# Performance work log

Hardware: AMD Instinct MI355X
Metric: run time of the kernel (lower is better)

## Reference

```python
import jax, jax.numpy as jnp
import numpy as np

B, N, CQ, CKV, CP = 4, 1024, 128, 64, 16
H, NB = 4, 3
D = CQ // H  # 32 per-head dim
NQ, NK = 32, 128
CENTRES = 15.5 + 32.0 * np.arange(N // NQ)  # subset centres covering all atoms


def _ln(x, eps=1e-5):
    m = jnp.mean(x, axis=-1, keepdims=True)
    v = jnp.var(x, axis=-1, keepdims=True)
    return (x - m) * jax.lax.rsqrt(v + eps)


def _adaln(a, s, s_gamma, w_gate, w_skip):
    # AF3 AdaLN: a normalized without affine, modulated by conditioning s
    a_n = _ln(a)
    s_n = _ln(s) * s_gamma
    return jax.nn.sigmoid(s_n @ w_gate) * a_n + s_n @ w_skip


def _local_bias():
    # sequence-local block mask (union over subset centres), Algorithm 7
    idx = jnp.arange(N, dtype=jnp.float32)
    cen = jnp.asarray(CENTRES, dtype=jnp.float32)
    lcond = jnp.abs(idx[None, :] - cen[:, None]) < NQ / 2  # [C, N] query window
    mcond = jnp.abs(idx[None, :] - cen[:, None]) < NK / 2  # [C, N] key window
    cond = jnp.any(lcond[:, :, None] & mcond[:, None, :], axis=0)  # [N, N]
    return jnp.where(cond, 0.0, -1e10)


def _forward(q, c, p, attn_s_gamma, attn_gate_w, attn_skip_w, attn_wq, attn_bq,
             attn_wk, attn_wv, attn_lnz_g, attn_lnz_b, attn_wb, attn_wgate,
             attn_wo, attn_ws_out, attn_bs_out, trans_s_gamma, trans_gate_w,
             trans_skip_w, trans_w1, trans_w2, trans_wout, trans_ws_out,
             trans_bs_out):
    beta = _local_bias()  # [N, N]
    inv_sqrt_d = 1.0 / np.sqrt(D)
    a = q
    for i in range(NB):  # 3 structurally distinct blocks
        # --- AttentionPairBias (AF3 Alg 24) ---
        ah = _adaln(a, c, attn_s_gamma[i], attn_gate_w[i], attn_skip_w[i])
        qh = (ah @ attn_wq[i] + attn_bq[i]).reshape(B, N, H, D)
        kh = (ah @ attn_wk[i]).reshape(B, N, H, D)
        vh = (ah @ attn_wv[i]).reshape(B, N, H, D)
        zb = (_ln(p) * attn_lnz_g[i] + attn_lnz_b[i]) @ attn_wb[i]  # [B,N,N,H]
        bias = jnp.transpose(zb, (0, 3, 1, 2)) + beta[None, None]  # [B,H,N,N]
        scores = jnp.einsum('bqhd,bkhd->bhqk', qh, kh) * inv_sqrt_d + bias
        w = jax.nn.softmax(scores, axis=-1)
        o = jnp.einsum('bhqk,bkhd->bqhd', w, vh)
        g = jax.nn.sigmoid((ah @ attn_wgate[i]).reshape(B, N, H, D))
        o = (g * o).reshape(B, N, CQ) @ attn_wo[i]
        attn_out = jax.nn.sigmoid(c @ attn_ws_out[i] + attn_bs_out[i]) * o
        # --- ConditionedTransitionBlock (AF3 Alg 25, n=2 SwiGLU) ---
        t = _adaln(a, c, trans_s_gamma[i], trans_gate_w[i], trans_skip_w[i])
        bm = jax.nn.silu(t @ trans_w1[i]) * (t @ trans_w2[i])
        t_out = jax.nn.sigmoid(c @ trans_ws_out[i] + trans_bs_out[i]) * (bm @ trans_wout[i])
        # AF3 Alg 23: a <- attn_out + transition(a, s)
        a = attn_out + t_out
    return a


def setup_inputs() -> dict:
    key = jax.random.key(0)
    ks = iter(jax.random.split(key, 64))

    def rnd(shape, scale=0.02):
        return jax.random.normal(next(ks), shape, dtype=jnp.float32) * scale

    return {
        'q': jax.random.normal(next(ks), (B, N, CQ), dtype=jnp.float32),
        'c': jax.random.normal(next(ks), (B, N, CKV), dtype=jnp.float32),
        'p': jax.random.normal(next(ks), (B, N, N, CP), dtype=jnp.float32),
        'attn_s_gamma': jnp.ones((NB, CKV), jnp.float32),
        'attn_gate_w': rnd((NB, CKV, CQ)),
        'attn_skip_w': rnd((NB, CKV, CQ)),
        'attn_wq': rnd((NB, CQ, CQ)),
        'attn_bq': jnp.zeros((NB, CQ), jnp.float32),
        'attn_wk': rnd((NB, CQ, CQ)),
        'attn_wv': rnd((NB, CQ, CQ)),
        'attn_lnz_g': jnp.ones((NB, CP), jnp.float32),
        'attn_lnz_b': jnp.zeros((NB, CP), jnp.float32),
        'attn_wb': rnd((NB, CP, H)),
        'attn_wgate': rnd((NB, CQ, CQ)),
        'attn_wo': rnd((NB, CQ, CQ)),
        'attn_ws_out': rnd((NB, CKV, CQ)),
        'attn_bs_out': jnp.full((NB, CQ), -2.0, jnp.float32),
        'trans_s_gamma': jnp.ones((NB, CKV), jnp.float32),
        'trans_gate_w': rnd((NB, CKV, CQ)),
        'trans_skip_w': rnd((NB, CKV, CQ)),
        'trans_w1': rnd((NB, CQ, 2 * CQ)),
        'trans_w2': rnd((NB, CQ, 2 * CQ)),
        'trans_wout': rnd((NB, 2 * CQ, CQ)),
        'trans_ws_out': rnd((NB, CKV, CQ)),
        'trans_bs_out': jnp.full((NB, CQ), -2.0, jnp.float32),
    }


def reference(q, c, p, attn_s_gamma, attn_gate_w, attn_skip_w, attn_wq, attn_bq,
              attn_wk, attn_wv, attn_lnz_g, attn_lnz_b, attn_wb, attn_wgate,
              attn_wo, attn_ws_out, attn_bs_out, trans_s_gamma, trans_gate_w,
              trans_skip_w, trans_w1, trans_w2, trans_wout, trans_ws_out,
              trans_bs_out):
    return _forward(q, c, p, attn_s_gamma, attn_gate_w, attn_skip_w, attn_wq,
                    attn_bq, attn_wk, attn_wv, attn_lnz_g, attn_lnz_b, attn_wb,
                    attn_wgate, attn_wo, attn_ws_out, attn_bs_out,
                    trans_s_gamma, trans_gate_w, trans_skip_w, trans_w1,
                    trans_w2, trans_wout, trans_ws_out, trans_bs_out)
```

## Files before the change

### kernel.cpp

```cpp
#include <hip/hip_runtime.h>
#include <math.h>

#define NB_ 3
#define B_ 4
#define N_ 1024
#define CQ_ 128
#define CKV_ 64
#define CP_ 16
#define H_ 4
#define D_ 32
#define R_ (B_*N_)
#define KW_ 128

__device__ __forceinline__ float sigmoidf_(float x) {
    return 1.0f / (1.0f + __expf(-x));
}

#define AN_OFF 0
#define SA_OFF 1056
#define ST_OFF 1600
#define CR_OFF 2144
#define TH_OFF 2688
#define SCR_OFF 3744
#define SMEM_F (3744 + 6336)

__global__ __launch_bounds__(512, 4) void k_pre(
    const float* __restrict__ a, const float* __restrict__ c,
    const float* __restrict__ a_sg, const float* __restrict__ a_gw,
    const float* __restrict__ a_sw, const float* __restrict__ a_wso,
    const float* __restrict__ a_bso,
    const float* __restrict__ t_sg, const float* __restrict__ t_gw,
    const float* __restrict__ t_sw, const float* __restrict__ t_wso,
    const float* __restrict__ t_bso,
    const float* __restrict__ wq, const float* __restrict__ bq,
    const float* __restrict__ wk, const float* __restrict__ wv,
    const float* __restrict__ wg,
    const float* __restrict__ w1, const float* __restrict__ w2,
    float* __restrict__ qh, float* __restrict__ kh,
    float* __restrict__ vh, float* __restrict__ gh,
    float* __restrict__ bm,
    float* __restrict__ asig, float* __restrict__ tsig)
{
    __shared__ float smem[SMEM_F];
    const int t = threadIdx.x;
    const int base = blockIdx.x * 8;

    {
        const int rloc = t >> 6, li = t & 63;
        const int row = base + rloc;
        float2 av = *(const float2*)(a + row * 128 + li * 2);
        float s = av.x + av.y;
        float ss = av.x * av.x + av.y * av.y;
        float cv = c[row * 64 + li];
        float cs = cv, css = cv * cv;
        #pragma unroll
        for (int m = 1; m < 64; m <<= 1) {
            s += __shfl_xor(s, m);
            ss += __shfl_xor(ss, m);
            cs += __shfl_xor(cs, m);
            css += __shfl_xor(css, m);
        }
        const float am = s * (1.0f / 128.0f);
        const float ars = rsqrtf(ss * (1.0f / 128.0f) - am * am + 1e-5f);
        const float cm = cs * (1.0f / 64.0f);
        const float crs = rsqrtf(css * (1.0f / 64.0f) - cm * cm + 1e-5f);
        smem[AN_OFF + rloc * 132 + li * 2]     = (av.x - am) * ars;
        smem[AN_OFF + rloc * 132 + li * 2 + 1] = (av.y - am) * ars;
        const float cn = (cv - cm) * crs;
        smem[SA_OFF + rloc * 68 + li] = cn * a_sg[li];
        smem[ST_OFF + rloc * 68 + li] = cn * t_sg[li];
        smem[CR_OFF + rloc * 68 + li] = cv;
    }
    __syncthreads();

    const int wave = t >> 6;
    const int lane = t & 63;
    const int ig = lane >> 4;
    const int jc = lane & 15;
    const int c0 = jc * 8;
    const int r0 = ig * 2, r1 = ig * 2 + 1;

    if (wave < 6) {
        const float* W;
        const float* xs;
        switch (wave) {
            case 0: W = a_gw;  xs = smem + SA_OFF; break;
            case 1: W = a_sw;  xs = smem + SA_OFF; break;
            case 2: W = t_gw;  xs = smem + ST_OFF; break;
            case 3: W = t_sw;  xs = smem + ST_OFF; break;
            case 4: W = a_wso; xs = smem + CR_OFF; break;
            default: W = t_wso; xs = smem + CR_OFF; break;
        }
        W += c0;
        float acc0[8], acc1[8];
        #pragma unroll
        for (int e = 0; e < 8; e++) { acc0[e] = 0.f; acc1[e] = 0.f; }
        for (int kk = 0; kk < 64; kk += 4) {
            float4 x40 = *(const float4*)(xs + r0 * 68 + kk);
            float4 x41 = *(const float4*)(xs + r1 * 68 + kk);
            #pragma unroll
            for (int q = 0; q < 4; q++) {
                const float4 wlo = *(const float4*)(W + (kk + q) * 128);
                const float4 whi = *(const float4*)(W + (kk + q) * 128 + 4);
                const float xa = ((const float*)&x40)[q];
                const float xb = ((const float*)&x41)[q];
                acc0[0] += xa * wlo.x; acc0[1] += xa * wlo.y;
                acc0[2] += xa * wlo.z; acc0[3] += xa * wlo.w;
                acc0[4] += xa * whi.x; acc0[5] += xa * whi.y;
                acc0[6] += xa * whi.z; acc0[7] += xa * whi.w;
                acc1[0] += xb * wlo.x; acc1[1] += xb * wlo.y;
                acc1[2] += xb * wlo.z; acc1[3] += xb * wlo.w;
                acc1[4] += xb * whi.x; acc1[5] += xb * whi.y;
                acc1[6] += xb * whi.z; acc1[7] += xb * whi.w;
            }
        }
        float* sc = smem + SCR_OFF + wave * 1056;
        *(float4*)(sc + r0 * 132 + c0)     = make_float4(acc0[0], acc0[1], acc0[2], acc0[3]);
        *(float4*)(sc + r0 * 132 + c0 + 4) = make_float4(acc0[4], acc0[5], acc0[6], acc0[7]);
        *(float4*)(sc + r1 * 132 + c0)     = make_float4(acc1[0], acc1[1], acc1[2], acc1[3]);
        *(float4*)(sc + r1 * 132 + c0 + 4) = make_float4(acc1[4], acc1[5], acc1[6], acc1[7]);
    }
    __syncthreads();

    #pragma unroll
    for (int i2 = 0; i2 < 2; i2++) {
        const int e = t + i2 * 512;
        const int r = e >> 7, cc = e & 127;
        const float* sc = smem + SCR_OFF + r * 132 + cc;
        const float anv = smem[AN_OFF + r * 132 + cc];
        const float ahv = sigmoidf_(sc[0]) * anv + sc[1056];
        const float thv = sigmoidf_(sc[2 * 1056]) * anv + sc[3 * 1056];
        smem[AN_OFF + r * 132 + cc] = ahv;
        smem[TH_OFF + r * 132 + cc] = thv;
        const int idx = (base + r) * 128 + cc;
        asig[idx] = sigmoidf_(sc[4 * 1056] + a_bso[cc]);
        tsig[idx] = sigmoidf_(sc[5 * 1056] + t_bso[cc]);
    }
    __syncthreads();

    {
        const float* W;
        const float* xs;
        int ldw, sel2 = 0, cb = 0;
        if (wave < 4) {
            W = (wave == 0 ? wq : wave == 1 ? wk : wave == 2 ? wv : wg) + c0;
            xs = smem + AN_OFF;
            ldw = 128;
        } else {
            const int u = (wave - 4) * 128 + c0;
            sel2 = u >> 8; cb = u & 255;
            W = (sel2 ? w2 : w1) + cb;
            xs = smem + TH_OFF;
            ldw = 256;
        }
        float acc0[8], acc1[8];
        #pragma unroll
        for (int e = 0; e < 8; e++) {
            const float init = (wave == 0) ? bq[c0 + e] : 0.f;
            acc0[e] = init; acc1[e] = init;
        }
        for (int kk = 0; kk < 128; kk += 4) {
            float4 x40 = *(const float4*)(xs + r0 * 132 + kk);
            float4 x41 = *(const float4*)(xs + r1 * 132 + kk);
            #pragma unroll
            for (int q = 0; q < 4; q++) {
                const float4 wlo = *(const float4*)(W + (kk + q) * ldw);
                const float4 whi = *(const float4*)(W + (kk + q) * ldw + 4);
                const float xa = ((const float*)&x40)[q];
                const float xb = ((const float*)&x41)[q];
                acc0[0] += xa * wlo.x; acc0[1] += xa * wlo.y;
                acc0[2] += xa * wlo.z; acc0[3] += xa * wlo.w;
                acc0[4] += xa * whi.x; acc0[5] += xa * whi.y;
                acc0[6] += xa * whi.z; acc0[7] += xa * whi.w;
                acc1[0] += xb * wlo.x; acc1[1] += xb * wlo.y;
                acc1[2] += xb * wlo.z; acc1[3] += xb * wlo.w;
                acc1[4] += xb * whi.x; acc1[5] += xb * whi.y;
                acc1[6] += xb * whi.z; acc1[7] += xb * whi.w;
            }
        }
        if (wave < 4) {
            float* dst = (wave == 0 ? qh : wave == 1 ? kh : wave == 2 ? vh : gh);
            if (wave == 3) {
                #pragma unroll
                for (int e = 0; e < 8; e++) {
                    acc0[e] = sigmoidf_(acc0[e]);
                    acc1[e] = sigmoidf_(acc1[e]);
                }
            }
            *(float4*)(dst + (base + r0) * 128 + c0)     = make_float4(acc0[0], acc0[1], acc0[2], acc0[3]);
            *(float4*)(dst + (base + r0) * 128 + c0 + 4) = make_float4(acc0[4], acc0[5], acc0[6], acc0[7]);
            *(float4*)(dst + (base + r1) * 128 + c0)     = make_float4(acc1[0], acc1[1], acc1[2], acc1[3]);
            *(float4*)(dst + (base + r1) * 128 + c0 + 4) = make_float4(acc1[4], acc1[5], acc1[6], acc1[7]);
        } else {
            float* bsc = smem + SCR_OFF + sel2 * 2080;
            *(float4*)(bsc + r0 * 260 + cb)     = make_float4(acc0[0], acc0[1], acc0[2], acc0[3]);
            *(float4*)(bsc + r0 * 260 + cb + 4) = make_float4(acc0[4], acc0[5], acc0[6], acc0[7]);
            *(float4*)(bsc + r1 * 260 + cb)     = make_float4(acc1[0], acc1[1], acc1[2], acc1[3]);
            *(float4*)(bsc + r1 * 260 + cb + 4) = make_float4(acc1[4], acc1[5], acc1[6], acc1[7]);
        }
    }
    __syncthreads();

    #pragma unroll
    for (int i2 = 0; i2 < 4; i2++) {
        const int e = t + i2 * 512;
        const int r = e >> 8, cc = e & 255;
        const float a1 = smem[SCR_OFF + r * 260 + cc];
        const float a2 = smem[SCR_OFF + 2080 + r * 260 + cc];
        bm[(base + r) * 256 + cc] = a1 * sigmoidf_(a1) * a2;
    }
}

__global__ __launch_bounds__(256) void k_zbias(
    const float* __restrict__ p,
    const float* __restrict__ lnz_g, const float* __restrict__ lnz_b,
    const float* __restrict__ wb, float* __restrict__ zb)
{
    const int tid = blockIdx.x * 256 + threadIdx.x;
    const int kk = tid & 127;
    const int n = (tid >> 7) & 1023;
    const int b = tid >> 17;
    const int row = b * N_ + n;
    const int k = ((n >> 5) << 5) - 48 + kk;

    if (k < 0 || k >= N_) {
        #pragma unroll
        for (int blk = 0; blk < NB_; blk++) {
            float* zo = zb + ((size_t)(blk * R_ + row) * H_) * KW_ + kk;
            #pragma unroll
            for (int h = 0; h < H_; h++) zo[h * KW_] = -1e10f;
        }
        return;
    }
    const float* pp = p + ((size_t)row * N_ + k) * CP_;
    float pv[16];
    float4 p0 = *(const float4*)(pp);
    float4 p1 = *(const float4*)(pp + 4);
    float4 p2 = *(const float4*)(pp + 8);
    float4 p3 = *(const float4*)(pp + 12);
    pv[0]=p0.x; pv[1]=p0.y; pv[2]=p0.z; pv[3]=p0.w;
    pv[4]=p1.x; pv[5]=p1.y; pv[6]=p1.z; pv[7]=p1.w;
    pv[8]=p2.x; pv[9]=p2.y; pv[10]=p2.z; pv[11]=p2.w;
    pv[12]=p3.x; pv[13]=p3.y; pv[14]=p3.z; pv[15]=p3.w;
    float s = 0.f, ss = 0.f;
    #pragma unroll
    for (int i = 0; i < 16; i++) { s += pv[i]; ss += pv[i] * pv[i]; }
    const float m = s * (1.0f / 16.0f);
    const float rs = rsqrtf(ss * (1.0f / 16.0f) - m * m + 1e-5f);

    #pragma unroll
    for (int blk = 0; blk < NB_; blk++) {
        const float* g = lnz_g + blk * 16;
        const float* bb = lnz_b + blk * 16;
        const float* w = wb + blk * 64;
        float z0 = 0.f, z1 = 0.f, z2 = 0.f, z3 = 0.f;
        #pragma unroll
        for (int cp = 0; cp < 16; cp++) {
            const float val = (pv[cp] - m) * rs * g[cp] + bb[cp];
            z0 += val * w[cp * 4 + 0];
            z1 += val * w[cp * 4 + 1];
            z2 += val * w[cp * 4 + 2];
            z3 += val * w[cp * 4 + 3];
        }
        float* zo = zb + ((size_t)(blk * R_ + row) * H_) * KW_ + kk;
        zo[0] = z0; zo[KW_] = z1; zo[2 * KW_] = z2; zo[3 * KW_] = z3;
    }
}

__global__ __launch_bounds__(256) void k_attn(
    const float* __restrict__ qh, const float* __restrict__ kh,
    const float* __restrict__ vh, const float* __restrict__ gh,
    const float* __restrict__ zb, float* __restrict__ og)
{
    __shared__ float kT[32][136];
    __shared__ float vs[128][36];
    __shared__ float wsm[32][132];

    const int t = threadIdx.x;
    const int qb = blockIdx.x, h = blockIdx.y, b = blockIdx.z;
    const int k0 = qb * 32 - 48;

    #pragma unroll
    for (int i = 0; i < 16; i++) {
        const int e = t + i * 256;
        const int kk = e >> 5, d = e & 31;
        const int kg = k0 + kk;
        float kvv = 0.f, vvv = 0.f;
        if (kg >= 0 && kg < N_) {
            const int addr = (b * N_ + kg) * 128 + h * 32 + d;
            kvv = kh[addr]; vvv = vh[addr];
        }
        kT[d][kk] = kvv;
        vs[kk][d] = vvv;
    }

    const int q = t >> 3, j = t & 7;
    const int n = qb * 32 + q;
    const float* qrow = qh + (b * N_ + n) * 128 + h * 32;
    float4 qf[8];
    #pragma unroll
    for (int dq = 0; dq < 8; dq++) qf[dq] = *(const float4*)(qrow + dq * 4);
    const float* zrow = zb + ((size_t)(b * N_ + n) * H_ + h) * KW_;
    float4 zf[4];
    #pragma unroll
    for (int g4 = 0; g4 < 4; g4++) zf[g4] = *(const float4*)(zrow + j * 16 + g4 * 4);
    __syncthreads();

    float4 acc[4];
    #pragma unroll
    for (int g4 = 0; g4 < 4; g4++) acc[g4] = make_float4(0.f, 0.f, 0.f, 0.f);
    const float* qfs = (const float*)qf;
    for (int d = 0; d < 32; d++) {
        const float qd = qfs[d];
        #pragma unroll
        for (int g4 = 0; g4 < 4; g4++) {
            const float4 k4 = *(const float4*)&kT[d][j * 16 + g4 * 4];
            acc[g4].x += qd * k4.x; acc[g4].y += qd * k4.y;
            acc[g4].z += qd * k4.z; acc[g4].w += qd * k4.w;
        }
    }
    const float scale = 0.1767766952966369f;
    float fr[16];
    #pragma unroll
    for (int g4 = 0; g4 < 4; g4++) {
        fr[g4*4+0] = zf[g4].x + acc[g4].x * scale;
        fr[g4*4+1] = zf[g4].y + acc[g4].y * scale;
        fr[g4*4+2] = zf[g4].z + acc[g4].z * scale;
        fr[g4*4+3] = zf[g4].w + acc[g4].w * scale;
    }
    float mx = fr[0];
    #pragma unroll
    for (int i = 1; i < 16; i++) mx = fmaxf(mx, fr[i]);
    #pragma unroll
    for (int mk = 1; mk < 8; mk <<= 1) mx = fmaxf(mx, __shfl_xor(mx, mk));
    float sum = 0.f;
    #pragma unroll
    for (int i = 0; i < 16; i++) { fr[i] = __expf(fr[i] - mx); sum += fr[i]; }
    #pragma unroll
    for (int mk = 1; mk < 8; mk <<= 1) sum += __shfl_xor(sum, mk);
    const float rinv = 1.0f / sum;
    #pragma unroll
    for (int g4 = 0; g4 < 4; g4++)
        #pragma unroll
        for (int mm = 0; mm < 4; mm++)
            wsm[q][j * 16 + g4 * 4 + mm] = fr[g4 * 4 + mm] * rinv;
    __syncthreads();

    const int q2 = t >> 3, dg = t & 7;
    float4 o = make_float4(0.f, 0.f, 0.f, 0.f);
    for (int kk = 0; kk < 128; kk++) {
        const float wv_ = wsm[q2][kk];
        const float4 v4 = *(const float4*)&vs[kk][dg * 4];
        o.x += wv_ * v4.x; o.y += wv_ * v4.y;
        o.z += wv_ * v4.z; o.w += wv_ * v4.w;
    }
    const int n2 = qb * 32 + q2;
    const int addr = (b * N_ + n2) * 128 + h * 32 + dg * 4;
    const float4 g4v = *(const float4*)(gh + addr);
    float4 outv;
    outv.x = o.x * g4v.x; outv.y = o.y * g4v.y;
    outv.z = o.z * g4v.z; outv.w = o.w * g4v.w;
    *(float4*)(og + addr) = outv;
}

__global__ __launch_bounds__(256, 4) void k_combine(
    const float* __restrict__ og, const float* __restrict__ bm,
    const float* __restrict__ wo, const float* __restrict__ wout,
    const float* __restrict__ asig, const float* __restrict__ tsig,
    float* __restrict__ out)
{
    __shared__ float scr[4 * 1056];
    const int t = threadIdx.x;
    const int base = blockIdx.x * 8;
    const int wave = t >> 6, lane = t & 63;
    const int ig = lane >> 4, jc = lane & 15;
    const int c0 = jc * 8;
    const int r0 = ig * 2, r1 = ig * 2 + 1;

    float acc0[8], acc1[8];
    #pragma unroll
    for (int e = 0; e < 8; e++) { acc0[e] = 0.f; acc1[e] = 0.f; }

    if (wave < 2) {
        const float* W = wo + c0;
        const float* X = og + base * 128;
        const int kbeg = wave * 64;
        for (int kk = kbeg; kk < kbeg + 64; kk += 4) {
            float4 x40 = *(const float4*)(X + r0 * 128 + kk);
            float4 x41 = *(const float4*)(X + r1 * 128 + kk);
            #pragma unroll
            for (int q = 0; q < 4; q++) {
                const float4 wlo = *(const float4*)(W + (kk + q) * 128);
                const float4 whi = *(const float4*)(W + (kk + q) * 128 + 4);
                const float xa = ((const float*)&x40)[q];
                const float xb = ((const float*)&x41)[q];
                acc0[0] += xa * wlo.x; acc0[1] += xa * wlo.y;
                acc0[2] += xa * wlo.z; acc0[3] += xa * wlo.w;
                acc0[4] += xa * whi.x; acc0[5] += xa * whi.y;
                acc0[6] += xa * whi.z; acc0[7] += xa * whi.w;
                acc1[0] += xb * wlo.x; acc1[1] += xb * wlo.y;
                acc1[2] += xb * wlo.z; acc1[3] += xb * wlo.w;
                acc1[4] += xb * whi.x; acc1[5] += xb * whi.y;
                acc1[6] += xb * whi.z; acc1[7] += xb * whi.w;
            }
        }
    } else {
        const float* W = wout + c0;
        const float* X = bm + base * 256;
        const int kbeg = (wave - 2) * 128;
        for (int kk = kbeg; kk < kbeg + 128; kk += 4) {
            float4 x40 = *(const float4*)(X + r0 * 256 + kk);
            float4 x41 = *(const float4*)(X + r1 * 256 + kk);
            #pragma unroll
            for (int q = 0; q < 4; q++) {
                const float4 wlo = *(const float4*)(W + (kk + q) * 128);
                const float4 whi = *(const float4*)(W + (kk + q) * 128 + 4);
                const float xa = ((const float*)&x40)[q];
                const float xb = ((const float*)&x41)[q];
                acc0[0] += xa * wlo.x; acc0[1] += xa * wlo.y;
                acc0[2] += xa * wlo.z; acc0[3] += xa * wlo.w;
                acc0[4] += xa * whi.x; acc0[5] += xa * whi.y;
                acc0[6] += xa * whi.z; acc0[7] += xa * whi.w;
                acc1[0] += xb * wlo.x; acc1[1] += xb * wlo.y;
                acc1[2] += xb * wlo.z; acc1[3] += xb * wlo.w;
                acc1[4] += xb * whi.x; acc1[5] += xb * whi.y;
                acc1[6] += xb * whi.z; acc1[7] += xb * whi.w;
            }
        }
    }
    float* sc = scr + wave * 1056;
    *(float4*)(sc + r0 * 132 + c0)     = make_float4(acc0[0], acc0[1], acc0[2], acc0[3]);
    *(float4*)(sc + r0 * 132 + c0 + 4) = make_float4(acc0[4], acc0[5], acc0[6], acc0[7]);
    *(float4*)(sc + r1 * 132 + c0)     = make_float4(acc1[0], acc1[1], acc1[2], acc1[3]);
    *(float4*)(sc + r1 * 132 + c0 + 4) = make_float4(acc1[4], acc1[5], acc1[6], acc1[7]);
    __syncthreads();

    #pragma unroll
    for (int i2 = 0; i2 < 4; i2++) {
        const int e = t + i2 * 256;
        const int r = e >> 7, cc = e & 127;
        const float* s = scr + r * 132 + cc;
        const int idx = (base + r) * 128 + cc;
        out[idx] = asig[idx] * (s[0] + s[1056]) + tsig[idx] * (s[2112] + s[3168]);
    }
}

extern "C" void kernel_launch(void* const* d_in, const int* in_sizes, int n_in,
                              void* d_out, int out_size, void* d_ws, size_t ws_size,
                              hipStream_t stream)
{
    const float* q        = (const float*)d_in[0];
    const float* c        = (const float*)d_in[1];
    const float* p        = (const float*)d_in[2];
    const float* a_sg_all = (const float*)d_in[3];
    const float* a_gw_all = (const float*)d_in[4];
    const float* a_sw_all = (const float*)d_in[5];
    const float* wq_all   = (const float*)d_in[6];
    const float* bq_all   = (const float*)d_in[7];
    const float* wk_all   = (const float*)d_in[8];
    const float* wv_all   = (const float*)d_in[9];
    const float* lnzg_all = (const float*)d_in[10];
    const float* lnzb_all = (const float*)d_in[11];
    const float* wb_all   = (const float*)d_in[12];
    const float* wgt_all  = (const float*)d_in[13];
    const float* wo_all   = (const float*)d_in[14];
    const float* awso_all = (const float*)d_in[15];
    const float* abso_all = (const float*)d_in[16];
    const float* t_sg_all = (const float*)d_in[17];
    const float* t_gw_all = (const float*)d_in[18];
    const float* t_sw_all = (const float*)d_in[19];
    const float* w1_all   = (const float*)d_in[20];
    const float* w2_all   = (const float*)d_in[21];
    const float* wout_all = (const float*)d_in[22];
    const float* twso_all = (const float*)d_in[23];
    const float* tbso_all = (const float*)d_in[24];

    float* ws = (float*)d_ws;
    const size_t RC = (size_t)R_ * CQ_;
    float* qh   = ws;
    float* kh   = ws + RC;
    float* vh   = ws + 2 * RC;
    float* gh   = ws + 3 * RC;
    float* bmb  = ws + 4 * RC;
    float* asig = ws + 6 * RC;
    float* tsig = ws + 7 * RC;
    float* abuf = ws + 8 * RC;
    float* ogb  = ws + 9 * RC;
    float* zbb  = ws + 10 * RC;

    k_zbias<<<dim3(B_ * N_ * KW_ / 256), dim3(256), 0, stream>>>(
        p, lnzg_all, lnzb_all, wb_all, zbb);

    const float* acur = q;
    for (int blk = 0; blk < NB_; blk++) {
        k_pre<<<dim3(R_ / 8), dim3(512), 0, stream>>>(
            acur, c,
            a_sg_all + blk * CKV_, a_gw_all + blk * CKV_ * CQ_,
            a_sw_all + blk * CKV_ * CQ_, awso_all + blk * CKV_ * CQ_,
            abso_all + blk * CQ_,
            t_sg_all + blk * CKV_, t_gw_all + blk * CKV_ * CQ_,
            t_sw_all + blk * CKV_ * CQ_, twso_all + blk * CKV_ * CQ_,
            tbso_all + blk * CQ_,
            wq_all + blk * CQ_ * CQ_, bq_all + blk * CQ_,
            wk_all + blk * CQ_ * CQ_, wv_all + blk * CQ_ * CQ_,
            wgt_all + blk * CQ_ * CQ_,
            w1_all + blk * CQ_ * 2 * CQ_, w2_all + blk * CQ_ * 2 * CQ_,
            qh, kh, vh, gh, bmb, asig, tsig);
        k_attn<<<dim3(N_ / 32, H_, B_), dim3(256), 0, stream>>>(
            qh, kh, vh, gh, zbb + (size_t)blk * R_ * H_ * KW_, ogb);
        float* outp = (blk == NB_ - 1) ? (float*)d_out : abuf;
        k_combine<<<dim3(R_ / 8), dim3(256), 0, stream>>>(
            ogb, bmb, wo_all + blk * CQ_ * CQ_, wout_all + blk * 2 * CQ_ * CQ_,
            asig, tsig, outp);
        acur = abuf;
    }
}
```

Baseline: 648.5 us.

## Fuse output combine with next block's prep, fold z-bias into first prep

The separate z-bias kernel is folded into a new first-block prep kernel. Each block's output projection and gating now run in one kernel, k_cp, with the next block's AdaLN and QKV/transition projections, so the intermediate activation never round-trips through global memory and fewer kernels are launched. The attention kernel moves to 512 threads with a flattened grid, stages Q in shared memory, loads K/V as vectors, and splits the weighted-V reduction across lane pairs. In exchange, the output projection in k_cp is a simple per-row loop, and bm, asig and tsig are read and rewritten in place under restrict pointers.

New measurement: 686.4 us. +5.8%, slower.

```diff
diff --git a/kernel.cpp b/kernel.cpp
--- a/kernel.cpp
+++ b/kernel.cpp
@@ -24,8 +24,9 @@
 #define SCR_OFF 3744
 #define SMEM_F (3744 + 6336)
 
-__global__ __launch_bounds__(512, 4) void k_pre(
-    const float* __restrict__ a, const float* __restrict__ c,
+__device__ __forceinline__ void pre_body(
+    float2 av, float* smem, int base,
+    const float* __restrict__ c,
     const float* __restrict__ a_sg, const float* __restrict__ a_gw,
     const float* __restrict__ a_sw, const float* __restrict__ a_wso,
     const float* __restrict__ a_bso,
@@ -41,14 +42,10 @@
     float* __restrict__ bm,
     float* __restrict__ asig, float* __restrict__ tsig)
 {
-    __shared__ float smem[SMEM_F];
     const int t = threadIdx.x;
-    const int base = blockIdx.x * 8;
-
     {
         const int rloc = t >> 6, li = t & 63;
         const int row = base + rloc;
-        float2 av = *(const float2*)(a + row * 128 + li * 2);
         float s = av.x + av.y;
         float ss = av.x * av.x + av.y * av.y;
         float cv = c[row * 64 + li];
@@ -99,11 +96,11 @@
             float4 x40 = *(const float4*)(xs + r0 * 68 + kk);
             float4 x41 = *(const float4*)(xs + r1 * 68 + kk);
             #pragma unroll
-            for (int q = 0; q < 4; q++) {
-                const float4 wlo = *(const float4*)(W + (kk + q) * 128);
-                const float4 whi = *(const float4*)(W + (kk + q) * 128 + 4);
-                const float xa = ((const float*)&x40)[q];
-                const float xb = ((const float*)&x41)[q];
+            for (int qq = 0; qq < 4; qq++) {
+                const float4 wlo = *(const float4*)(W + (kk + qq) * 128);
+                const float4 whi = *(const float4*)(W + (kk + qq) * 128 + 4);
+                const float xa = ((const float*)&x40)[qq];
+                const float xb = ((const float*)&x41)[qq];
                 acc0[0] += xa * wlo.x; acc0[1] += xa * wlo.y;
                 acc0[2] += xa * wlo.z; acc0[3] += xa * wlo.w;
                 acc0[4] += xa * whi.x; acc0[5] += xa * whi.y;
@@ -163,11 +160,11 @@
             float4 x40 = *(const float4*)(xs + r0 * 132 + kk);
             float4 x41 = *(const float4*)(xs + r1 * 132 + kk);
             #pragma unroll
-            for (int q = 0; q < 4; q++) {
-                const float4 wlo = *(const float4*)(W + (kk + q) * ldw);
-                const float4 whi = *(const float4*)(W + (kk + q) * ldw + 4);
-                const float xa = ((const float*)&x40)[q];
-                const float xb = ((const float*)&x41)[q];
+            for (int qq = 0; qq < 4; qq++) {
+                const float4 wlo = *(const float4*)(W + (kk + qq) * ldw);
+                const float4 whi = *(const float4*)(W + (kk + qq) * ldw + 4);
+                const float xa = ((const float*)&x40)[qq];
+                const float xb = ((const float*)&x41)[qq];
                 acc0[0] += xa * wlo.x; acc0[1] += xa * wlo.y;
                 acc0[2] += xa * wlo.z; acc0[3] += xa * wlo.w;
                 acc0[4] += xa * whi.x; acc0[5] += xa * whi.y;
@@ -211,237 +208,255 @@
     }
 }
 
-__global__ __launch_bounds__(256) void k_zbias(
+__global__ __launch_bounds__(512, 4) void k_pre0(
+    const float* __restrict__ a, const float* __restrict__ c,
     const float* __restrict__ p,
     const float* __restrict__ lnz_g, const float* __restrict__ lnz_b,
-    const float* __restrict__ wb, float* __restrict__ zb)
+    const float* __restrict__ wb, float* __restrict__ zb,
+    const float* __restrict__ a_sg, const float* __restrict__ a_gw,
+    const float* __restrict__ a_sw, const float* __restrict__ a_wso,
+    const float* __restrict__ a_bso,
+    const float* __restrict__ t_sg, const float* __restrict__ t_gw,
+    const float* __restrict__ t_sw, const float* __restrict__ t_wso,
+    const float* __restrict__ t_bso,
+    const float* __restrict__ wq, const float* __restrict__ bq,
+    const float* __restrict__ wk, const float* __restrict__ wv,
+    const float* __restrict__ wg,
+    const float* __restrict__ w1, const float* __restrict__ w2,
+    float* __restrict__ qh, float* __restrict__ kh,
+    float* __restrict__ vh, float* __restrict__ gh,
+    float* __restrict__ bm,
+    float* __restrict__ asig, float* __restrict__ tsig)
 {
-    const int tid = blockIdx.x * 256 + threadIdx.x;
-    const int kk = tid & 127;
-    const int n = (tid >> 7) & 1023;
-    const int b = tid >> 17;
-    const int row = b * N_ + n;
-    const int k = ((n >> 5) << 5) - 48 + kk;
-
-    if (k < 0 || k >= N_) {
-        #pragma unroll
-        for (int blk = 0; blk < NB_; blk++) {
-            float* zo = zb + ((size_t)(blk * R_ + row) * H_) * KW_ + kk;
+    __shared__ float smem[SMEM_F];
+    const int t = threadIdx.x;
+    const int base = blockIdx.x * 8;
+
+    #pragma unroll
+    for (int i = 0; i < 2; i++) {
+        const int e = t + i * 512;
+        const int r = e >> 7, kk = e & 127;
+        const int row = base + r;
+        const int n = row & 1023;
+        const int k = ((n >> 5) << 5) - 48 + kk;
+        if (k < 0 || k >= N_) {
             #pragma unroll
-            for (int h = 0; h < H_; h++) zo[h * KW_] = -1e10f;
-        }
+            for (int blk = 0; blk < NB_; blk++) {
+                float* zo = zb + ((size_t)(blk * R_ + row) * H_) * KW_ + kk;
+                #pragma unroll
+                for (int h = 0; h < H_; h++) zo[h * KW_] = -1e10f;
+            }
+        } else {
+            const float* pp = p + ((size_t)row * N_ + k) * CP_;
+            float pv[16];
+            float4 p0 = *(const float4*)(pp);
+            float4 p1 = *(const float4*)(pp + 4);
+            float4 p2 = *(const float4*)(pp + 8);
+            float4 p3 = *(const float4*)(pp + 12);
+            pv[0]=p0.x; pv[1]=p0.y; pv[2]=p0.z; pv[3]=p0.w;
+            pv[4]=p1.x; pv[5]=p1.y; pv[6]=p1.z; pv[7]=p1.w;
+            pv[8]=p2.x; pv[9]=p2.y; pv[10]=p2.z; pv[11]=p2.w;
+            pv[12]=p3.x; pv[13]=p3.y; pv[14]=p3.z; pv[15]=p3.w;
+            float s = 0.f, ss = 0.f;
+            #pragma unroll
+            for (int ii = 0; ii < 16; ii++) { s += pv[ii]; ss += pv[ii] * pv[ii]; }
+            const float m = s * (1.0f / 16.0f);
+            const float rs = rsqrtf(ss * (1.0f / 16.0f) - m * m + 1e-5f);
+            #pragma unroll
+            for (int blk = 0; blk < NB_; blk++) {
+                const float* g = lnz_g + blk * 16;
+                const float* bb = lnz_b + blk * 16;
+                const float* w = wb + blk * 64;
+                float z0 = 0.f, z1 = 0.f, z2 = 0.f, z3 = 0.f;
+                #pragma unroll
+                for (int cp = 0; cp < 16; cp++) {
+                    const float val = (pv[cp] - m) * rs * g[cp] + bb[cp];
+                    z0 += val * w[cp * 4 + 0];
+                    z1 += val * w[cp * 4 + 1];
+                    z2 += val * w[cp * 4 + 2];
+                    z3 += val * w[cp * 4 + 3];
+                }
+                float* zo = zb + ((size_t)(blk * R_ + row) * H_) * KW_ + kk;
+                zo[0] = z0; zo[KW_] = z1; zo[2 * KW_] = z2; zo[3 * KW_] = z3;
+            }
+        }
+    }
+
+    float2 av = *(const float2*)(a + (base + (t >> 6)) * 128 + (t & 63) * 2);
+    pre_body(av, smem, base, c, a_sg, a_gw, a_sw, a_wso, a_bso,
+             t_sg, t_gw, t_sw, t_wso, t_bso, wq, bq, wk, wv, wg, w1, w2,
+             qh, kh, vh, gh, bm, asig, tsig);
+}
+
+__global__ __launch_bounds__(512, 4) void k_cp(
+    const float* __restrict__ og, const float* __restrict__ bm_in,
+    const float* __restrict__ wo, const float* __restrict__ wout,
+    const float* __restrict__ asig_in, const float* __restrict__ tsig_in,
+    float* __restrict__ out_final, int final_,
+    const float* __restrict__ c,
+    const float* __restrict__ a_sg, const float* __restrict__ a_gw,
+    const float* __restrict__ a_sw, const float* __restrict__ a_wso,
+    const float* __restrict__ a_bso,
+    const float* __restrict__ t_sg, const float* __restrict__ t_gw,
+    const float* __restrict__ t_sw, const float* __restrict__ t_wso,
+    const float* __restrict__ t_bso,
+    const float* __restrict__ wq, const float* __restrict__ bq,
+    const float* __restrict__ wk, const float* __restrict__ wv,
+    const float* __restrict__ wg,
+    const float* __restrict__ w1, const float* __restrict__ w2,
+    float* __restrict__ qh, float* __restrict__ kh,
+    float* __restrict__ vh, float* __restrict__ gh,
+    float* __restrict__ bm,
+    float* __restrict__ asig, float* __restrict__ tsig)
+{
+    __shared__ float smem[SMEM_F];
+    float* ogs = smem + SCR_OFF;
+    float* bms = smem + SCR_OFF + 1056;
+    const int t = threadIdx.x;
+    const int base = blockIdx.x * 8;
+
+    if (t < 256) {
+        const int r = t >> 5, c4 = t & 31;
+        *(float4*)(ogs + r * 132 + c4 * 4) =
+            *(const float4*)(og + (base + r) * 128 + c4 * 4);
+    }
+    {
+        const int r = t >> 6, c4 = t & 63;
+        *(float4*)(bms + r * 260 + c4 * 4) =
+            *(const float4*)(bm_in + (base + r) * 256 + c4 * 4);
+    }
+    __syncthreads();
+
+    const int w = t >> 6, l = t & 63;
+    const int row = base + w;
+    float2 acc1 = make_float2(0.f, 0.f), acc2 = make_float2(0.f, 0.f);
+    for (int k = 0; k < 128; k++) {
+        const float x = ogs[w * 132 + k];
+        const float2 wv = *(const float2*)(wo + k * 128 + l * 2);
+        acc1.x += x * wv.x; acc1.y += x * wv.y;
+    }
+    for (int k = 0; k < 256; k++) {
+        const float x = bms[w * 260 + k];
+        const float2 wv = *(const float2*)(wout + k * 128 + l * 2);
+        acc2.x += x * wv.x; acc2.y += x * wv.y;
+    }
+    const float2 as = *(const float2*)(asig_in + row * 128 + l * 2);
+    const float2 ts = *(const float2*)(tsig_in + row * 128 + l * 2);
+    float2 outv;
+    outv.x = as.x * acc1.x + ts.x * acc2.x;
+    outv.y = as.y * acc1.y + ts.y * acc2.y;
+
+    if (final_) {
+        *(float2*)(out_final + row * 128 + l * 2) = outv;
         return;
     }
-    const float* pp = p + ((size_t)row * N_ + k) * CP_;
-    float pv[16];
-    float4 p0 = *(const float4*)(pp);
-    float4 p1 = *(const float4*)(pp + 4);
-    float4 p2 = *(const float4*)(pp + 8);
-    float4 p3 = *(const float4*)(pp + 12);
-    pv[0]=p0.x; pv[1]=p0.y; pv[2]=p0.z; pv[3]=p0.w;
-    pv[4]=p1.x; pv[5]=p1.y; pv[6]=p1.z; pv[7]=p1.w;
-    pv[8]=p2.x; pv[9]=p2.y; pv[10]=p2.z; pv[11]=p2.w;
-    pv[12]=p3.x; pv[13]=p3.y; pv[14]=p3.z; pv[15]=p3.w;
-    float s = 0.f, ss = 0.f;
-    #pragma unroll
-    for (int i = 0; i < 16; i++) { s += pv[i]; ss += pv[i] * pv[i]; }
-    const float m = s * (1.0f / 16.0f);
-    const float rs = rsqrtf(ss * (1.0f / 16.0f) - m * m + 1e-5f);
-
-    #pragma unroll
-    for (int blk = 0; blk < NB_; blk++) {
-        const float* g = lnz_g + blk * 16;
-        const float* bb = lnz_b + blk * 16;
-        const float* w = wb + blk * 64;
-        float z0 = 0.f, z1 = 0.f, z2 = 0.f, z3 = 0.f;
-        #pragma unroll
-        for (int cp = 0; cp < 16; cp++) {
-            const float val = (pv[cp] - m) * rs * g[cp] + bb[cp];
-            z0 += val * w[cp * 4 + 0];
-            z1 += val * w[cp * 4 + 1];
-            z2 += val * w[cp * 4 + 2];
-            z3 += val * w[cp * 4 + 3];
-        }
-        float* zo = zb + ((size_t)(blk * R_ + row) * H_) * KW_ + kk;
-        zo[0] = z0; zo[KW_] = z1; zo[2 * KW_] = z2; zo[3 * KW_] = z3;
-    }
+    pre_body(outv, smem, base, c, a_sg, a_gw, a_sw, a_wso, a_bso,
+             t_sg, t_gw, t_sw, t_wso, t_bso, wq, bq, wk, wv, wg, w1, w2,
+             qh, kh, vh, gh, bm, asig, tsig);
 }
 
-__global__ __launch_bounds__(256) void k_attn(
+__global__ __launch_bounds__(512, 4) void k_attn(
     const float* __restrict__ qh, const float* __restrict__ kh,
     const float* __restrict__ vh, const float* __restrict__ gh,
     const float* __restrict__ zb, float* __restrict__ og)
 {
-    __shared__ float kT[32][136];
-    __shared__ float vs[128][36];
-    __shared__ float wsm[32][132];
+    __shared__ float qs[32 * 36];
+    __shared__ float kT[32 * 136];
+    __shared__ float vs[128 * 36];
+    __shared__ float wsm[32 * 132];
 
     const int t = threadIdx.x;
-    const int qb = blockIdx.x, h = blockIdx.y, b = blockIdx.z;
+    const int qb = blockIdx.x & 31;
+    const int h = (blockIdx.x >> 5) & 3;
+    const int b = blockIdx.x >> 7;
     const int k0 = qb * 32 - 48;
 
     #pragma unroll
-    for (int i = 0; i < 16; i++) {
-        const int e = t + i * 256;
-        const int kk = e >> 5, d = e & 31;
+    for (int i = 0; i < 2; i++) {
+        const int e = t + i * 512;
+        const int kk = e >> 3, dq = e & 7;
         const int kg = k0 + kk;
-        float kvv = 0.f, vvv = 0.f;
+        float4 kv = make_float4(0.f, 0.f, 0.f, 0.f);
+        float4 vv = make_float4(0.f, 0.f, 0.f, 0.f);
         if (kg >= 0 && kg < N_) {
-            const int addr = (b * N_ + kg) * 128 + h * 32 + d;
-            kvv = kh[addr]; vvv = vh[addr];
-        }
-        kT[d][kk] = kvv;
-        vs[kk][d] = vvv;
-    }
-
-    const int q = t >> 3, j = t & 7;
+            const int addr = (b * N_ + kg) * 128 + h * 32 + dq * 4;
+            kv = *(const float4*)(kh + addr);
+            vv = *(const float4*)(vh + addr);
+        }
+        kT[(dq * 4 + 0) * 136 + kk] = kv.x;
+        kT[(dq * 4 + 1) * 136 + kk] = kv.y;
+        kT[(dq * 4 + 2) * 136 + kk] = kv.z;
+        kT[(dq * 4 + 3) * 136 + kk] = kv.w;
+        *(float4*)(vs + kk * 36 + dq * 4) = vv;
+    }
+    if (t < 256) {
+        const int q = t >> 3, dq = t & 7;
+        const int n = qb * 32 + q;
+        *(float4*)(qs + q * 36 + dq * 4) =
+            *(const float4*)(qh + (b * N_ + n) * 128 + h * 32 + dq * 4);
+    }
+    const int q = t >> 4, jj = t & 15;
     const int n = qb * 32 + q;
-    const float* qrow = qh + (b * N_ + n) * 128 + h * 32;
-    float4 qf[8];
-    #pragma unroll
-    for (int dq = 0; dq < 8; dq++) qf[dq] = *(const float4*)(qrow + dq * 4);
     const float* zrow = zb + ((size_t)(b * N_ + n) * H_ + h) * KW_;
-    float4 zf[4];
-    #pragma unroll
-    for (int g4 = 0; g4 < 4; g4++) zf[g4] = *(const float4*)(zrow + j * 16 + g4 * 4);
-    __syncthreads();
-
-    float4 acc[4];
-    #pragma unroll
-    for (int g4 = 0; g4 < 4; g4++) acc[g4] = make_float4(0.f, 0.f, 0.f, 0.f);
-    const float* qfs = (const float*)qf;
+    const float4 z0 = *(const float4*)(zrow + jj * 8);
+    const float4 z1 = *(const float4*)(zrow + jj * 8 + 4);
+    __syncthreads();
+
+    float acc[8];
+    #pragma unroll
+    for (int e = 0; e < 8; e++) acc[e] = 0.f;
     for (int d = 0; d < 32; d++) {
-        const float qd = qfs[d];
-        #pragma unroll
-        for (int g4 = 0; g4 < 4; g4++) {
-            const float4 k4 = *(const float4*)&kT[d][j * 16 + g4 * 4];
-            acc[g4].x += qd * k4.x; acc[g4].y += qd * k4.y;
-            acc[g4].z += qd * k4.z; acc[g4].w += qd * k4.w;
-        }
+        const float qv = qs[q * 36 + d];
+        const float4 ka = *(const float4*)(kT + d * 136 + jj * 8);
+        const float4 kb = *(const float4*)(kT + d * 136 + jj * 8 + 4);
+        acc[0] += qv * ka.x; acc[1] += qv * ka.y;
+        acc[2] += qv * ka.z; acc[3] += qv * ka.w;
+        acc[4] += qv * kb.x; acc[5] += qv * kb.y;
+        acc[6] += qv * kb.z; acc[7] += qv * kb.w;
     }
     const float scale = 0.1767766952966369f;
-    float fr[16];
-    #pragma unroll
-    for (int g4 = 0; g4 < 4; g4++) {
-        fr[g4*4+0] = zf[g4].x + acc[g4].x * scale;
-        fr[g4*4+1] = zf[g4].y + acc[g4].y * scale;
-        fr[g4*4+2] = zf[g4].z + acc[g4].z * scale;
-        fr[g4*4+3] = zf[g4].w + acc[g4].w * scale;
-    }
+    float fr[8];
+    fr[0] = acc[0] * scale + z0.x; fr[1] = acc[1] * scale + z0.y;
+    fr[2] = acc[2] * scale + z0.z; fr[3] = acc[3] * scale + z0.w;
+    fr[4] = acc[4] * scale + z1.x; fr[5] = acc[5] * scale + z1.y;
+    fr[6] = acc[6] * scale + z1.z; fr[7] = acc[7] * scale + z1.w;
     float mx = fr[0];
     #pragma unroll
-    for (int i = 1; i < 16; i++) mx = fmaxf(mx, fr[i]);
-    #pragma unroll
-    for (int mk = 1; mk < 8; mk <<= 1) mx = fmaxf(mx, __shfl_xor(mx, mk));
+    for (int i = 1; i < 8; i++) mx = fmaxf(mx, fr[i]);
+    #pragma unroll
+    for (int mk = 1; mk < 16; mk <<= 1) mx = fmaxf(mx, __shfl_xor(mx, mk));
     float sum = 0.f;
     #pragma unroll
-    for (int i = 0; i < 16; i++) { fr[i] = __expf(fr[i] - mx); sum += fr[i]; }
-    #pragma unroll
-    for (int mk = 1; mk < 8; mk <<= 1) sum += __shfl_xor(sum, mk);
+    for (int i = 0; i < 8; i++) { fr[i] = __expf(fr[i] - mx); sum += fr[i]; }
+    #pragma unroll
+    for (int mk = 1; mk < 16; mk <<= 1) sum += __shfl_xor(sum, mk);
     const float rinv = 1.0f / sum;
     #pragma unroll
-    for (int g4 = 0; g4 < 4; g4++)
-        #pragma unroll
-        for (int mm = 0; mm < 4; mm++)
-            wsm[q][j * 16 + g4 * 4 + mm] = fr[g4 * 4 + mm] * rinv;
-    __syncthreads();
-
-    const int q2 = t >> 3, dg = t & 7;
+    for (int i = 0; i < 8; i++)
+        wsm[q * 132 + jj * 8 + i] = fr[i] * rinv;
+    __syncthreads();
+
+    const int q2 = t >> 4, dq2 = (t >> 1) & 7, kh2 = t & 1;
     float4 o = make_float4(0.f, 0.f, 0.f, 0.f);
-    for (int kk = 0; kk < 128; kk++) {
-        const float wv_ = wsm[q2][kk];
-        const float4 v4 = *(const float4*)&vs[kk][dg * 4];
-        o.x += wv_ * v4.x; o.y += wv_ * v4.y;
-        o.z += wv_ * v4.z; o.w += wv_ * v4.w;
-    }
-    const int n2 = qb * 32 + q2;
-    const int addr = (b * N_ + n2) * 128 + h * 32 + dg * 4;
-    const float4 g4v = *(const float4*)(gh + addr);
-    float4 outv;
-    outv.x = o.x * g4v.x; outv.y = o.y * g4v.y;
-    outv.z = o.z * g4v.z; outv.w = o.w * g4v.w;
-    *(float4*)(og + addr) = outv;
-}
-
-__global__ __launch_bounds__(256, 4) void k_combine(
-    const float* __restrict__ og, const float* __restrict__ bm,
-    const float* __restrict__ wo, const float* __restrict__ wout,
-    const float* __restrict__ asig, const float* __restrict__ tsig,
-    float* __restrict__ out)
-{
-    __shared__ float scr[4 * 1056];
-    const int t = threadIdx.x;
-    const int base = blockIdx.x * 8;
-    const int wave = t >> 6, lane = t & 63;
-    const int ig = lane >> 4, jc = lane & 15;
-    const int c0 = jc * 8;
-    const int r0 = ig * 2, r1 = ig * 2 + 1;
-
-    float acc0[8], acc1[8];
-    #pragma unroll
-    for (int e = 0; e < 8; e++) { acc0[e] = 0.f; acc1[e] = 0.f; }
-
-    if (wave < 2) {
-        const float* W = wo + c0;
-        const float* X = og + base * 128;
-        const int kbeg = wave * 64;
-        for (int kk = kbeg; kk < kbeg + 64; kk += 4) {
-            float4 x40 = *(const float4*)(X + r0 * 128 + kk);
-            float4 x41 = *(const float4*)(X + r1 * 128 + kk);
-            #pragma unroll
-            for (int q = 0; q < 4; q++) {
-                const float4 wlo = *(const float4*)(W + (kk + q) * 128);
-                const float4 whi = *(const float4*)(W + (kk + q) * 128 + 4);
-                const float xa = ((const float*)&x40)[q];
-                const float xb = ((const float*)&x41)[q];
-                acc0[0] += xa * wlo.x; acc0[1] += xa * wlo.y;
-                acc0[2] += xa * wlo.z; acc0[3] += xa * wlo.w;
-                acc0[4] += xa * whi.x; acc0[5] += xa * whi.y;
-                acc0[6] += xa * whi.z; acc0[7] += xa * whi.w;
-                acc1[0] += xb * wlo.x; acc1[1] += xb * wlo.y;
-                acc1[2] += xb * wlo.z; acc1[3] += xb * wlo.w;
-                acc1[4] += xb * whi.x; acc1[5] += xb * whi.y;
-                acc1[6] += xb * whi.z; acc1[7] += xb * whi.w;
-            }
-        }
-    } else {
-        const float* W = wout + c0;
-        const float* X = bm + base * 256;
-        const int kbeg = (wave - 2) * 128;
-        for (int kk = kbeg; kk < kbeg + 128; kk += 4) {
-            float4 x40 = *(const float4*)(X + r0 * 256 + kk);
-            float4 x41 = *(const float4*)(X + r1 * 256 + kk);
-            #pragma unroll
-            for (int q = 0; q < 4; q++) {
-                const float4 wlo = *(const float4*)(W + (kk + q) * 128);
-                const float4 whi = *(const float4*)(W + (kk + q) * 128 + 4);
-                const float xa = ((const float*)&x40)[q];
-                const float xb = ((const float*)&x41)[q];
-                acc0[0] += xa * wlo.x; acc0[1] += xa * wlo.y;
-                acc0[2] += xa * wlo.z; acc0[3] += xa * wlo.w;
-                acc0[4] += xa * whi.x; acc0[5] += xa * whi.y;
-                acc0[6] += xa * whi.z; acc0[7] += xa * whi.w;
-                acc1[0] += xb * wlo.x; acc1[1] += xb * wlo.y;
-                acc1[2] += xb * wlo.z; acc1[3] += xb * wlo.w;
-                acc1[4] += xb * whi.x; acc1[5] += xb * whi.y;
-                acc1[6] += xb * whi.z; acc1[7] += xb * whi.w;
-            }
-        }
-    }
-    float* sc = scr + wave * 1056;
-    *(float4*)(sc + r0 * 132 + c0)     = make_float4(acc0[0], acc0[1], acc0[2], acc0[3]);
-    *(float4*)(sc + r0 * 132 + c0 + 4) = make_float4(acc0[4], acc0[5], acc0[6], acc0[7]);
-    *(float4*)(sc + r1 * 132 + c0)     = make_float4(acc1[0], acc1[1], acc1[2], acc1[3]);
-    *(float4*)(sc + r1 * 132 + c0 + 4) = make_float4(acc1[4], acc1[5], acc1[6], acc1[7]);
-    __syncthreads();
-
-    #pragma unroll
-    for (int i2 = 0; i2 < 4; i2++) {
-        const int e = t + i2 * 256;
-        const int r = e >> 7, cc = e & 127;
-        const float* s = scr + r * 132 + cc;
-        const int idx = (base + r) * 128 + cc;
-        out[idx] = asig[idx] * (s[0] + s[1056]) + tsig[idx] * (s[2112] + s[3168]);
+    const int kbeg = kh2 * 64;
+    for (int kk = kbeg; kk < kbeg + 64; kk++) {
+        const float wv = wsm[q2 * 132 + kk];
+        const float4 v4 = *(const float4*)(vs + kk * 36 + dq2 * 4);
+        o.x += wv * v4.x; o.y += wv * v4.y;
+        o.z += wv * v4.z; o.w += wv * v4.w;
+    }
+    o.x += __shfl_xor(o.x, 1);
+    o.y += __shfl_xor(o.y, 1);
+    o.z += __shfl_xor(o.z, 1);
+    o.w += __shfl_xor(o.w, 1);
+    if (kh2 == 0) {
+        const int n2 = qb * 32 + q2;
+        const int addr = (b * N_ + n2) * 128 + h * 32 + dq2 * 4;
+        const float4 g4 = *(const float4*)(gh + addr);
+        float4 outv;
+        outv.x = o.x * g4.x; outv.y = o.y * g4.y;
+        outv.z = o.z * g4.z; outv.w = o.w * g4.w;
+        *(float4*)(og + addr) = outv;
     }
 }
 
@@ -484,34 +499,36 @@
     float* bmb  = ws + 4 * RC;
     float* asig = ws + 6 * RC;
     float* tsig = ws + 7 * RC;
-    float* abuf = ws + 8 * RC;
-    float* ogb  = ws + 9 * RC;
-    float* zbb  = ws + 10 * RC;
-
-    k_zbias<<<dim3(B_ * N_ * KW_ / 256), dim3(256), 0, stream>>>(
-        p, lnzg_all, lnzb_all, wb_all, zbb);
-
-    const float* acur = q;
+    float* ogb  = ws + 8 * RC;
+    float* zbb  = ws + 9 * RC;
+
+    k_pre0<<<dim3(R_ / 8), dim3(512), 0, stream>>>(
+        q, c, p, lnzg_all, lnzb_all, wb_all, zbb,
+        a_sg_all, a_gw_all, a_sw_all, awso_all, abso_all,
+        t_sg_all, t_gw_all, t_sw_all, twso_all, tbso_all,
+        wq_all, bq_all, wk_all, wv_all, wgt_all, w1_all, w2_all,
+        qh, kh, vh, gh, bmb, asig, tsig);
+
     for (int blk = 0; blk < NB_; blk++) {
-        k_pre<<<dim3(R_ / 8), dim3(512), 0, stream>>>(
-            acur, c,
-            a_sg_all + blk * CKV_, a_gw_all + blk * CKV_ * CQ_,
-            a_sw_all + blk * CKV_ * CQ_, awso_all + blk * CKV_ * CQ_,
-            abso_all + blk * CQ_,
-            t_sg_all + blk * CKV_, t_gw_all + blk * CKV_ * CQ_,
-            t_sw_all + blk * CKV_ * CQ_, twso_all + blk * CKV_ * CQ_,
-            tbso_all + blk * CQ_,
-            wq_all + blk * CQ_ * CQ_, bq_all + blk * CQ_,
-            wk_all + blk * CQ_ * CQ_, wv_all + blk * CQ_ * CQ_,
-            wgt_all + blk * CQ_ * CQ_,
-            w1_all + blk * CQ_ * 2 * CQ_, w2_all + blk * CQ_ * 2 * CQ_,
+        k_attn<<<dim3(512), dim3(512), 0, stream>>>(
+            qh, kh, vh, gh, zbb + (size_t)blk * R_ * H_ * KW_, ogb);
+        const int nxt = blk + 1;
+        const int fin = (nxt == NB_);
+        const int wi = fin ? 0 : nxt;
+        k_cp<<<dim3(R_ / 8), dim3(512), 0, stream>>>(
+            ogb, bmb, wo_all + blk * CQ_ * CQ_, wout_all + blk * 2 * CQ_ * CQ_,
+            asig, tsig, (float*)d_out, fin,
+            c,
+            a_sg_all + wi * CKV_, a_gw_all + wi * CKV_ * CQ_,
+            a_sw_all + wi * CKV_ * CQ_, awso_all + wi * CKV_ * CQ_,
+            abso_all + wi * CQ_,
+            t_sg_all + wi * CKV_, t_gw_all + wi * CKV_ * CQ_,
+            t_sw_all + wi * CKV_ * CQ_, twso_all + wi * CKV_ * CQ_,
+            tbso_all + wi * CQ_,
+            wq_all + wi * CQ_ * CQ_, bq_all + wi * CQ_,
+            wk_all + wi * CQ_ * CQ_, wv_all + wi * CQ_ * CQ_,
+            wgt_all + wi * CQ_ * CQ_,
+            w1_all + wi * CQ_ * 2 * CQ_, w2_all + wi * CQ_ * 2 * CQ_,
             qh, kh, vh, gh, bmb, asig, tsig);
-        k_attn<<<dim3(N_ / 32, H_, B_), dim3(256), 0, stream>>>(
-            qh, kh, vh, gh, zbb + (size_t)blk * R_ * H_ * KW_, ogb);
-        float* outp = (blk == NB_ - 1) ? (float*)d_out : abuf;
-        k_combine<<<dim3(R_ / 8), dim3(256), 0, stream>>>(
-            ogb, bmb, wo_all + blk * CQ_ * CQ_, wout_all + blk * 2 * CQ_ * CQ_,
-            asig, tsig, outp);
-        acur = abuf;
     }
 }
```
